# Performance work log

Hardware: AMD Instinct MI355X
Metric: run time of the kernel (lower is better)

## Reference

```python
import jax, jax.numpy as jnp
import numpy as np

N = 16384
INPUT_DIM = 256
HIDDEN1 = 128
HIDDEN2 = 64


def setup_inputs() -> dict:
    key = jax.random.key(0)
    ks = jax.random.split(key, 8)
    X = jax.random.normal(ks[0], (N, INPUT_DIM), dtype=jnp.float32)
    adj = jax.random.uniform(ks[1], (N, N), dtype=jnp.float32)
    # Xavier-uniform style scaling for weights
    def xavier(k, shape):
        fan_in, fan_out = shape
        lim = float(np.sqrt(6.0 / (fan_in + fan_out)))
        return jax.random.uniform(k, shape, dtype=jnp.float32, minval=-lim, maxval=lim)
    W1 = xavier(ks[2], (INPUT_DIM, HIDDEN1))
    Wm = xavier(ks[3], (HIDDEN1, HIDDEN2))
    Ws = xavier(ks[4], (HIDDEN1, HIDDEN2))
    Wp = xavier(ks[5], (HIDDEN2, HIDDEN2))
    bp = jnp.zeros((HIDDEN2,), dtype=jnp.float32)
    noise = jax.random.normal(ks[6], (N, HIDDEN2), dtype=jnp.float32)
    return {"X": X, "adj": adj, "W1": W1, "Wm": Wm, "Ws": Ws,
            "Wp": Wp, "bp": bp, "noise": noise}


def _gcn(x, adj, W, activation):
    # GraphConvSparse: adj @ (x @ W) then activation
    h = adj @ (x @ W)
    return activation(h)


def reference(X, adj, W1, Wm, Ws, Wp, bp, noise):
    # base GCN with ReLU
    hidden = _gcn(X, adj, W1, jax.nn.relu)            # [N, hidden1]
    # mean branch: identity-activation GCN then Linear projection
    Z = _gcn(hidden, adj, Wm, lambda x: x)            # [N, hidden2]
    mean = Z @ Wp + bp                                # [N, hidden2]
    # logstd branch with clamp(max=10)
    logstd = _gcn(hidden, adj, Ws, lambda x: x)
    logstd = jnp.minimum(logstd, 10.0)
    # reparameterization trick
    sampled_z = noise * jnp.exp(logstd) + mean        # [N, hidden2]
    return sampled_z
```

## Files before the change

kernel.cpp:

```cpp
#include <hip/hip_runtime.h>


typedef __bf16 bf16_t;
typedef __attribute__((ext_vector_type(4))) __bf16 bf16x4;
typedef __attribute__((ext_vector_type(8))) __bf16 bf16x8;
typedef __attribute__((ext_vector_type(16))) float f32x16;
typedef __attribute__((ext_vector_type(4)))  float f32x4;

#define N_NODES 16384
#define MFMA3(ACC, A, B) \
    ACC = __builtin_amdgcn_mfma_f32_32x32x16_bf16(A, B, ACC, 0, 0, 0)

__device__ __forceinline__ int frag_off(int r, int c) {
    int K16  = r >> 4;
    int cblk = c >> 5;
    int g    = (r >> 3) & 1;
    int lane = (c & 31) + (g << 5);
    return ((K16 * 4 + cblk) << 9) + (lane << 3) + (r & 7);
}

__device__ __forceinline__ float4 relu_add4(float4 a, float4 b) {
    float4 r;
    r.x = fmaxf(a.x + b.x, 0.f); r.y = fmaxf(a.y + b.y, 0.f);
    r.z = fmaxf(a.z + b.z, 0.f); r.w = fmaxf(a.w + b.w, 0.f);
    return r;
}

template<int K, bool FUSED, bool ADD2>
__global__ __launch_bounds__(256)
void producer_kernel(const float* __restrict__ A,
                     const float* __restrict__ A2,
                     const float* __restrict__ W,
                     const float* __restrict__ Wa,
                     const float* __restrict__ Wb,
                     bf16_t* __restrict__ Bh,
                     bf16_t* __restrict__ Bl)
{
    __shared__ float As[32][128];
    __shared__ float Wsh[32][128];
    const int t    = threadIdx.x;
    const int row0 = blockIdx.x * 128;
    const int tc   = t & 15, tr = t >> 4;

    float acc[8][8];
    #pragma unroll
    for (int i = 0; i < 8; ++i)
        #pragma unroll
        for (int j = 0; j < 8; ++j) acc[i][j] = 0.f;

    const int ra = t >> 1, ks = (t & 1) << 4;
    const int wk = t >> 3, wc = (t & 7) << 4;

    for (int k0 = 0; k0 < K; k0 += 32) {
        const float* ap = A + (size_t)(row0 + ra) * K + k0 + ks;
        float4 a0 = *(const float4*)(ap);
        float4 a1 = *(const float4*)(ap + 4);
        float4 a2 = *(const float4*)(ap + 8);
        float4 a3 = *(const float4*)(ap + 12);
        if (ADD2) {
            const float* ap2 = A2 + (size_t)(row0 + ra) * K + k0 + ks;
            a0 = relu_add4(a0, *(const float4*)(ap2));
            a1 = relu_add4(a1, *(const float4*)(ap2 + 4));
            a2 = relu_add4(a2, *(const float4*)(ap2 + 8));
            a3 = relu_add4(a3, *(const float4*)(ap2 + 12));
        }
        float4 w0, w1, w2, w3;
        if (!FUSED) {
            const float* wp = W + (size_t)(k0 + wk) * 128 + wc;
            w0 = *(const float4*)(wp);     w1 = *(const float4*)(wp + 4);
            w2 = *(const float4*)(wp + 8); w3 = *(const float4*)(wp + 12);
        } else {
            const float* wp = (wc < 64) ? (Wa + (size_t)(k0 + wk) * 64 + wc)
                                        : (Wb + (size_t)(k0 + wk) * 64 + (wc - 64));
            w0 = *(const float4*)(wp);     w1 = *(const float4*)(wp + 4);
            w2 = *(const float4*)(wp + 8); w3 = *(const float4*)(wp + 12);
        }
        __syncthreads();
        {
            float tmp[16] = {a0.x,a0.y,a0.z,a0.w, a1.x,a1.y,a1.z,a1.w,
                             a2.x,a2.y,a2.z,a2.w, a3.x,a3.y,a3.z,a3.w};
            #pragma unroll
            for (int j = 0; j < 16; ++j) As[ks + j][ra] = tmp[j];
            *(float4*)&Wsh[wk][wc     ] = w0;
            *(float4*)&Wsh[wk][wc +  4] = w1;
            *(float4*)&Wsh[wk][wc +  8] = w2;
            *(float4*)&Wsh[wk][wc + 12] = w3;
        }
        __syncthreads();
        #pragma unroll 4
        for (int k = 0; k < 32; ++k) {
            float av[8], wv[8];
            *(float4*)&av[0] = *(const float4*)&As[k][8 * tr];
            *(float4*)&av[4] = *(const float4*)&As[k][8 * tr + 4];
            *(float4*)&wv[0] = *(const float4*)&Wsh[k][8 * tc];
            *(float4*)&wv[4] = *(const float4*)&Wsh[k][8 * tc + 4];
            #pragma unroll
            for (int i = 0; i < 8; ++i)
                #pragma unroll
                for (int j = 0; j < 8; ++j)
                    acc[i][j] = fmaf(av[i], wv[j], acc[i][j]);
        }
    }

    #pragma unroll
    for (int i = 0; i < 8; ++i) {
        int r = row0 + 8 * tr + i;
        #pragma unroll
        for (int j = 0; j < 8; ++j) {
            int c = 8 * tc + j;
            float v = acc[i][j];
            bf16_t h = (bf16_t)v;
            bf16_t l = (bf16_t)(v - (float)h);
            int off = frag_off(r, c);
            Bh[off] = h;
            Bl[off] = l;
        }
    }
}

struct BSet { bf16x8 h[4]; bf16x8 l[4]; };

__global__ __launch_bounds__(256, 4)
void adj_gemm_kernel(const float* __restrict__ adj,
                     const bf16_t* __restrict__ Bh,
                     const bf16_t* __restrict__ Bl,
                     float* __restrict__ P0,
                     float* __restrict__ P1)
{
    __shared__ __align__(16) bf16_t AsH[32 * 256];
    __shared__ __align__(16) bf16_t AsL[32 * 256];
    const int t    = threadIdx.x;
    const int lane = t & 63;
    const int w    = t >> 6;
    const int mt   = blockIdx.x >> 1;
    const int kh   = blockIdx.x & 1;
    const int row0 = mt << 5;
    const int hi32 = lane >> 5;
    float* const outP = kh ? P1 : P0;

    const float* aBase = adj + (size_t)(row0 + (w << 3)) * 16384
                             + (kh << 13) + (lane << 2);

    int wIdx[8];
    #pragma unroll
    for (int j = 0; j < 8; ++j) {
        int row = (w << 3) + j;
        wIdx[j] = (row << 8) + ((((lane >> 2) ^ (row & 15)) << 4)
                                + ((lane & 3) << 2));
    }

    const int frow  = lane & 31;
    const int rbase = (frow << 8) + (hi32 << 3);
    const int rx    = frow & 15;

    const int tb   = (w << 9) + (lane << 3);
    const int sub0 = kh << 7;

    f32x16 acc;
    #pragma unroll
    for (int i = 0; i < 16; ++i) acc[i] = 0.f;

    f32x4 ar[8];
    BSet S;

    auto loadAdj = [&](int mac) {
        const float* p = aBase + (mac << 8);
        #pragma unroll
        for (int j = 0; j < 8; ++j)
            ar[j] = __builtin_nontemporal_load((const f32x4*)(p + (size_t)j * 16384));
    };
    auto cvtWrite = [&]() {
        #pragma unroll
        for (int j = 0; j < 8; ++j) {
            bf16x4 hv, lv;
            #pragma unroll
            for (int e = 0; e < 4; ++e) {
                float v = ar[j][e];
                bf16_t h = (bf16_t)v;
                hv[e] = h;
                lv[e] = (bf16_t)(v - (float)h);
            }
            *(bf16x4*)&AsH[wIdx[j]] = hv;
            *(bf16x4*)&AsL[wIdx[j]] = lv;
        }
    };
    auto loadB = [&](int sub) {
        const size_t base = ((size_t)sub << 13) + tb;
        #pragma unroll
        for (int s = 0; s < 4; ++s) {
            S.h[s] = *(const bf16x8*)(Bh + base + (s << 11));
            S.l[s] = *(const bf16x8*)(Bl + base + (s << 11));
        }
    };
    auto computeS = [&](int s) {
        #pragma unroll
        for (int k16 = 0; k16 < 4; ++k16) {
            const int u  = (s << 2) + k16;
            const int id = rbase + ((u ^ rx) << 4);
            bf16x8 ah = *(const bf16x8*)&AsH[id];
            bf16x8 al = *(const bf16x8*)&AsL[id];
            MFMA3(acc, ah, S.h[k16]);
            MFMA3(acc, ah, S.l[k16]);
            MFMA3(acc, al, S.h[k16]);
        }
    };

#define SYNC_LDS() do { asm volatile("s_waitcnt lgkmcnt(0)" ::: "memory"); \
                        __builtin_amdgcn_s_barrier(); } while (0)

    loadAdj(0);
    for (int m = 0; m < 32; ++m) {
        cvtWrite();
        SYNC_LDS();
        const int sb = sub0 + (m << 2);
        loadB(sb + 0);
        if (m < 31) loadAdj(m + 1);
        computeS(0);
        loadB(sb + 1);  computeS(1);
        loadB(sb + 2);  computeS(2);
        loadB(sb + 3);  computeS(3);
        SYNC_LDS();
    }
#undef SYNC_LDS

    const int col = (w << 5) + (lane & 31);
    const int rb  = row0 + (hi32 << 2);
    #pragma unroll
    for (int q = 0; q < 16; ++q) {
        int r = rb + (q & 3) + ((q >> 2) << 3);
        outP[(size_t)r * 128 + col] = acc[q];
    }
}

__global__ __launch_bounds__(256)
void final_kernel(const float* __restrict__ T0,
                  const float* __restrict__ T1,
                  const float* __restrict__ Wp,
                  const float* __restrict__ bp,
                  const float* __restrict__ noise,
                  float* __restrict__ out)
{
    __shared__ float Wps[64][64];
    __shared__ float Ts[64][64];
    const int t = threadIdx.x;
    const int row0 = blockIdx.x * 64;
    {
        int k = t >> 2, c0 = (t & 3) << 4;
        #pragma unroll
        for (int i = 0; i < 4; ++i)
            *(float4*)&Wps[k][c0 + 4 * i] = *(const float4*)&Wp[(size_t)k * 64 + c0 + 4 * i];
        #pragma unroll
        for (int i = 0; i < 4; ++i) {
            float4 z0 = *(const float4*)&T0[(size_t)(row0 + k) * 128 + c0 + 4 * i];
            float4 z1 = *(const float4*)&T1[(size_t)(row0 + k) * 128 + c0 + 4 * i];
            float4 zs; zs.x = z0.x + z1.x; zs.y = z0.y + z1.y;
            zs.z = z0.z + z1.z; zs.w = z0.w + z1.w;
            *(float4*)&Ts[k][c0 + 4 * i] = zs;
        }
    }
    __syncthreads();

    const int r  = t >> 2;
    const int c0 = (t & 3) << 4;
    float acc[16];
    #pragma unroll
    for (int j = 0; j < 16; ++j) acc[j] = bp[c0 + j];
    for (int k = 0; k < 64; ++k) {
        float a = Ts[r][k];
        #pragma unroll
        for (int j = 0; j < 16; ++j) acc[j] = fmaf(a, Wps[k][c0 + j], acc[j]);
    }
    const int grow = row0 + r;
    #pragma unroll
    for (int j = 0; j < 16; ++j) {
        size_t li = (size_t)grow * 128 + 64 + c0 + j;
        float ls = T0[li] + T1[li];
        ls = fminf(ls, 10.0f);
        out[(size_t)grow * 64 + c0 + j] =
            noise[(size_t)grow * 64 + c0 + j] * __expf(ls) + acc[j];
    }
}

extern "C" void kernel_launch(void* const* d_in, const int* in_sizes, int n_in,
                              void* d_out, int out_size, void* d_ws, size_t ws_size,
                              hipStream_t stream) {
    const float* X     = (const float*)d_in[0];
    const float* adj   = (const float*)d_in[1];
    const float* W1    = (const float*)d_in[2];
    const float* Wm    = (const float*)d_in[3];
    const float* Wsv   = (const float*)d_in[4];
    const float* Wp    = (const float*)d_in[5];
    const float* bp    = (const float*)d_in[6];
    const float* noise = (const float*)d_in[7];
    float* out = (float*)d_out;

    char* ws = (char*)d_ws;
    bf16_t* Bh = (bf16_t*)ws;
    bf16_t* Bl = (bf16_t*)(ws + (4u << 20));
    float*  P0 = (float*)(ws + (8u << 20));
    float*  P1 = (float*)(ws + (16u << 20));

    producer_kernel<256, false, false><<<128, 256, 0, stream>>>(
        X, nullptr, W1, nullptr, nullptr, Bh, Bl);
    adj_gemm_kernel<<<1024, 256, 0, stream>>>(adj, Bh, Bl, P0, P1);
    producer_kernel<128, true, true><<<128, 256, 0, stream>>>(
        P0, P1, nullptr, Wm, Wsv, Bh, Bl);
    adj_gemm_kernel<<<1024, 256, 0, stream>>>(adj, Bh, Bl, P0, P1);
    final_kernel<<<256, 256, 0, stream>>>(P0, P1, Wp, bp, noise, out);
}
```

Before: 714.6 us.

## Enlarge adj GEMM row tile to 128 with 512-thread blocks and B reuse

The adjacency GEMM block now covers 128 rows instead of 32 and uses 8 waves. Each wave computes two 32-row accumulators that share the same B fragments, which halves B global loads per MFMA, and B register sets are double-buffered. The cost is more LDS (128 KB for the A tiles), higher register pressure, only 256 blocks (one per CU on 256 CUs), and lower occupancy, which can hurt latency hiding on the memory-bound adj stream.

```diff
diff --git a/kernel.cpp b/kernel.cpp
--- a/kernel.cpp
+++ b/kernel.cpp
@@ -120,58 +120,60 @@
 
 struct BSet { bf16x8 h[4]; bf16x8 l[4]; };
 
-__global__ __launch_bounds__(256, 4)
+__global__ __launch_bounds__(512, 2)
 void adj_gemm_kernel(const float* __restrict__ adj,
                      const bf16_t* __restrict__ Bh,
                      const bf16_t* __restrict__ Bl,
                      float* __restrict__ P0,
                      float* __restrict__ P1)
 {
-    __shared__ __align__(16) bf16_t AsH[32 * 256];
-    __shared__ __align__(16) bf16_t AsL[32 * 256];
+    __shared__ __align__(16) bf16_t AsH[128 * 256];
+    __shared__ __align__(16) bf16_t AsL[128 * 256];
     const int t    = threadIdx.x;
     const int lane = t & 63;
     const int w    = t >> 6;
     const int mt   = blockIdx.x >> 1;
     const int kh   = blockIdx.x & 1;
-    const int row0 = mt << 5;
+    const int row0 = mt << 7;
     const int hi32 = lane >> 5;
     float* const outP = kh ? P1 : P0;
 
-    const float* aBase = adj + (size_t)(row0 + (w << 3)) * 16384
+    const float* aBase = adj + (size_t)(row0 + (w << 4)) * 16384
                              + (kh << 13) + (lane << 2);
 
-    int wIdx[8];
-    #pragma unroll
-    for (int j = 0; j < 8; ++j) {
-        int row = (w << 3) + j;
+    int wIdx[16];
+    #pragma unroll
+    for (int j = 0; j < 16; ++j) {
+        int row = (w << 4) + j;
         wIdx[j] = (row << 8) + ((((lane >> 2) ^ (row & 15)) << 4)
                                 + ((lane & 3) << 2));
     }
 
-    const int frow  = lane & 31;
-    const int rbase = (frow << 8) + (hi32 << 3);
-    const int rx    = frow & 15;
-
-    const int tb   = (w << 9) + (lane << 3);
+    const int rh   = w >> 2, cq = w & 3;
+    const int frow = (rh << 6) + (lane & 31);
+    const int rbase0 = (frow << 8) + (hi32 << 3);
+    const int rbase1 = ((frow + 32) << 8) + (hi32 << 3);
+    const int rx     = frow & 15;
+
+    const int tb   = (cq << 9) + (lane << 3);
     const int sub0 = kh << 7;
 
-    f32x16 acc;
-    #pragma unroll
-    for (int i = 0; i < 16; ++i) acc[i] = 0.f;
-
-    f32x4 ar[8];
-    BSet S;
+    f32x16 acc0, acc1;
+    #pragma unroll
+    for (int i = 0; i < 16; ++i) { acc0[i] = 0.f; acc1[i] = 0.f; }
+
+    f32x4 ar[16];
+    BSet S0, S1;
 
     auto loadAdj = [&](int mac) {
         const float* p = aBase + (mac << 8);
         #pragma unroll
-        for (int j = 0; j < 8; ++j)
+        for (int j = 0; j < 16; ++j)
             ar[j] = __builtin_nontemporal_load((const f32x4*)(p + (size_t)j * 16384));
     };
     auto cvtWrite = [&]() {
         #pragma unroll
-        for (int j = 0; j < 8; ++j) {
+        for (int j = 0; j < 16; ++j) {
             bf16x4 hv, lv;
             #pragma unroll
             for (int e = 0; e < 4; ++e) {
@@ -184,7 +186,7 @@
             *(bf16x4*)&AsL[wIdx[j]] = lv;
         }
     };
-    auto loadB = [&](int sub) {
+    auto loadB = [&](BSet& S, int sub) {
         const size_t base = ((size_t)sub << 13) + tb;
         #pragma unroll
         for (int s = 0; s < 4; ++s) {
@@ -192,16 +194,21 @@
             S.l[s] = *(const bf16x8*)(Bl + base + (s << 11));
         }
     };
-    auto computeS = [&](int s) {
+    auto computeS = [&](const BSet& S, int s) {
         #pragma unroll
         for (int k16 = 0; k16 < 4; ++k16) {
             const int u  = (s << 2) + k16;
-            const int id = rbase + ((u ^ rx) << 4);
-            bf16x8 ah = *(const bf16x8*)&AsH[id];
-            bf16x8 al = *(const bf16x8*)&AsL[id];
-            MFMA3(acc, ah, S.h[k16]);
-            MFMA3(acc, ah, S.l[k16]);
-            MFMA3(acc, al, S.h[k16]);
+            const int o  = (u ^ rx) << 4;
+            bf16x8 ah0 = *(const bf16x8*)&AsH[rbase0 + o];
+            bf16x8 al0 = *(const bf16x8*)&AsL[rbase0 + o];
+            bf16x8 ah1 = *(const bf16x8*)&AsH[rbase1 + o];
+            bf16x8 al1 = *(const bf16x8*)&AsL[rbase1 + o];
+            MFMA3(acc0, ah0, S.h[k16]);
+            MFMA3(acc1, ah1, S.h[k16]);
+            MFMA3(acc0, ah0, S.l[k16]);
+            MFMA3(acc1, ah1, S.l[k16]);
+            MFMA3(acc0, al0, S.h[k16]);
+            MFMA3(acc1, al1, S.h[k16]);
         }
     };
 
@@ -213,22 +220,23 @@
         cvtWrite();
         SYNC_LDS();
         const int sb = sub0 + (m << 2);
-        loadB(sb + 0);
+        loadB(S0, sb + 0);
         if (m < 31) loadAdj(m + 1);
-        computeS(0);
-        loadB(sb + 1);  computeS(1);
-        loadB(sb + 2);  computeS(2);
-        loadB(sb + 3);  computeS(3);
+        computeS(S0, 0);
+        loadB(S1, sb + 1);  computeS(S1, 1);
+        loadB(S0, sb + 2);  computeS(S0, 2);
+        loadB(S1, sb + 3);  computeS(S1, 3);
         SYNC_LDS();
     }
 #undef SYNC_LDS
 
-    const int col = (w << 5) + (lane & 31);
-    const int rb  = row0 + (hi32 << 2);
+    const int col = (cq << 5) + (lane & 31);
+    const int rw  = row0 + (rh << 6) + (hi32 << 2);
     #pragma unroll
     for (int q = 0; q < 16; ++q) {
-        int r = rb + (q & 3) + ((q >> 2) << 3);
-        outP[(size_t)r * 128 + col] = acc[q];
+        int r = rw + (q & 3) + ((q >> 2) << 3);
+        outP[(size_t)r * 128 + col]        = acc0[q];
+        outP[(size_t)(r + 32) * 128 + col] = acc1[q];
     }
 }
 
@@ -302,9 +310,9 @@
 
     producer_kernel<256, false, false><<<128, 256, 0, stream>>>(
         X, nullptr, W1, nullptr, nullptr, Bh, Bl);
-    adj_gemm_kernel<<<1024, 256, 0, stream>>>(adj, Bh, Bl, P0, P1);
+    adj_gemm_kernel<<<256, 512, 0, stream>>>(adj, Bh, Bl, P0, P1);
     producer_kernel<128, true, true><<<128, 256, 0, stream>>>(
         P0, P1, nullptr, Wm, Wsv, Bh, Bl);
-    adj_gemm_kernel<<<1024, 256, 0, stream>>>(adj, Bh, Bl, P0, P1);
+    adj_gemm_kernel<<<256, 512, 0, stream>>>(adj, Bh, Bl, P0, P1);
     final_kernel<<<256, 256, 0, stream>>>(P0, P1, Wp, bp, noise, out);
 }
```

After: 726.7 us. About the same (+1.7%).

## Stage adjacency tiles via direct global-to-LDS loads with smaller K chunks

Applied to the files above, without the earlier changes.

Adjacency fp32 tiles now go straight into an LDS staging buffer through global_load_lds, and are then converted to bf16 hi/lo split buffers, instead of passing through registers. The K chunk per iteration is halved (128 instead of 256) and the loop count doubled. Both B sets for a chunk are loaded before compute. This is meant to cut register pressure and VGPR traffic from the prefetch. In exchange it adds an explicit vmcnt(0) wait each iteration, which can expose global latency because only one stage is buffered.

```diff
diff --git a/kernel.cpp b/kernel.cpp
--- a/kernel.cpp
+++ b/kernel.cpp
@@ -10,6 +10,10 @@
 #define N_NODES 16384
 #define MFMA3(ACC, A, B) \
     ACC = __builtin_amdgcn_mfma_f32_32x32x16_bf16(A, B, ACC, 0, 0, 0)
+
+#define GLOAD16(gp, lp) __builtin_amdgcn_global_load_lds(                    \
+    (const __attribute__((address_space(1))) unsigned int*)(gp),             \
+    (__attribute__((address_space(3))) unsigned int*)(lp), 16, 0, 0)
 
 __device__ __forceinline__ int frag_off(int r, int c) {
     int K16  = r >> 4;
@@ -127,8 +131,9 @@
                      float* __restrict__ P0,
                      float* __restrict__ P1)
 {
-    __shared__ __align__(16) bf16_t AsH[32 * 256];
-    __shared__ __align__(16) bf16_t AsL[32 * 256];
+    __shared__ __align__(16) float  Fst[32 * 128];
+    __shared__ __align__(16) bf16_t AsH[32 * 128];
+    __shared__ __align__(16) bf16_t AsL[32 * 128];
     const int t    = threadIdx.x;
     const int lane = t & 63;
     const int w    = t >> 6;
@@ -138,53 +143,48 @@
     const int hi32 = lane >> 5;
     float* const outP = kh ? P1 : P0;
 
-    const float* aBase = adj + (size_t)(row0 + (w << 3)) * 16384
-                             + (kh << 13) + (lane << 2);
-
-    int wIdx[8];
-    #pragma unroll
-    for (int j = 0; j < 8; ++j) {
-        int row = (w << 3) + j;
-        wIdx[j] = (row << 8) + ((((lane >> 2) ^ (row & 15)) << 4)
-                                + ((lane & 3) << 2));
-    }
-
-    const int frow  = lane & 31;
-    const int rbase = (frow << 8) + (hi32 << 3);
-    const int rx    = frow & 15;
-
-    const int tb   = (w << 9) + (lane << 3);
-    const int sub0 = kh << 7;
+    const char* gB = (const char*)adj
+                   + ((size_t)(row0 + (w << 3) + hi32) << 16)
+                   + (kh << 15) + ((lane & 31) << 4);
+
+    const int fr = lane & 31, rx = fr & 15;
+    const int tb = (w << 9) + (lane << 3);
 
     f32x16 acc;
     #pragma unroll
     for (int i = 0; i < 16; ++i) acc[i] = 0.f;
 
-    f32x4 ar[8];
-    BSet S;
-
-    auto loadAdj = [&](int mac) {
-        const float* p = aBase + (mac << 8);
-        #pragma unroll
-        for (int j = 0; j < 8; ++j)
-            ar[j] = __builtin_nontemporal_load((const f32x4*)(p + (size_t)j * 16384));
+    BSet S0, S1;
+
+    auto gload = [&](int mac) {
+        const char* p = gB + ((size_t)mac << 9);
+        #pragma unroll
+        for (int j = 0; j < 4; ++j)
+            GLOAD16(p + ((size_t)j << 17),
+                    (char*)Fst + (((w << 3) + 2 * j) << 9));
     };
-    auto cvtWrite = [&]() {
-        #pragma unroll
-        for (int j = 0; j < 8; ++j) {
+    auto cvt = [&]() {
+        #pragma unroll
+        for (int p = 0; p < 4; ++p) {
+            const int b = (w << 12) + (p << 10) + (lane << 4);
+            f32x4 v = *(const f32x4*)((const char*)Fst + b);
+            const int r    = (w << 3) + 2 * p + hi32;
+            const int g    = (lane & 31) >> 1;
+            const int half = lane & 1;
+            const int ob   = (r << 8) + (((g ^ (r & 15)) << 4) + (half << 3));
             bf16x4 hv, lv;
             #pragma unroll
             for (int e = 0; e < 4; ++e) {
-                float v = ar[j][e];
-                bf16_t h = (bf16_t)v;
+                float x = v[e];
+                bf16_t h = (bf16_t)x;
                 hv[e] = h;
-                lv[e] = (bf16_t)(v - (float)h);
+                lv[e] = (bf16_t)(x - (float)h);
             }
-            *(bf16x4*)&AsH[wIdx[j]] = hv;
-            *(bf16x4*)&AsL[wIdx[j]] = lv;
+            *(bf16x4*)((char*)AsH + ob) = hv;
+            *(bf16x4*)((char*)AsL + ob) = lv;
         }
     };
-    auto loadB = [&](int sub) {
+    auto loadB = [&](BSet& S, int sub) {
         const size_t base = ((size_t)sub << 13) + tb;
         #pragma unroll
         for (int s = 0; s < 4; ++s) {
@@ -192,13 +192,13 @@
             S.l[s] = *(const bf16x8*)(Bl + base + (s << 11));
         }
     };
-    auto computeS = [&](int s) {
+    auto computeS = [&](const BSet& S, int s) {
         #pragma unroll
         for (int k16 = 0; k16 < 4; ++k16) {
             const int u  = (s << 2) + k16;
-            const int id = rbase + ((u ^ rx) << 4);
-            bf16x8 ah = *(const bf16x8*)&AsH[id];
-            bf16x8 al = *(const bf16x8*)&AsL[id];
+            const int ob = (fr << 8) + (((((u << 1) + hi32) ^ rx)) << 4);
+            bf16x8 ah = *(const bf16x8*)((const char*)AsH + ob);
+            bf16x8 al = *(const bf16x8*)((const char*)AsL + ob);
             MFMA3(acc, ah, S.h[k16]);
             MFMA3(acc, ah, S.l[k16]);
             MFMA3(acc, al, S.h[k16]);
@@ -208,17 +208,17 @@
 #define SYNC_LDS() do { asm volatile("s_waitcnt lgkmcnt(0)" ::: "memory"); \
                         __builtin_amdgcn_s_barrier(); } while (0)
 
-    loadAdj(0);
-    for (int m = 0; m < 32; ++m) {
-        cvtWrite();
+    gload(0);
+    for (int m = 0; m < 64; ++m) {
+        asm volatile("s_waitcnt vmcnt(0)" ::: "memory");
+        cvt();
         SYNC_LDS();
-        const int sb = sub0 + (m << 2);
-        loadB(sb + 0);
-        if (m < 31) loadAdj(m + 1);
-        computeS(0);
-        loadB(sb + 1);  computeS(1);
-        loadB(sb + 2);  computeS(2);
-        loadB(sb + 3);  computeS(3);
+        const int sb = (kh << 7) + (m << 1);
+        loadB(S0, sb);
+        loadB(S1, sb + 1);
+        if (m < 63) gload(m + 1);
+        computeS(S0, 0);
+        computeS(S1, 1);
         SYNC_LDS();
     }
 #undef SYNC_LDS
```

New measurement: 795.4 us. 1.11x slower.
